# Kernel optimization log

Hardware: AMD Instinct MI355X
Metric: run time of the kernel (lower is better)

The kernel has to match this reference:

```python
import jax, jax.numpy as jnp
import numpy as np

N = 262144  # capacity (number of stored key/value rows)
D = 512     # key/query dim
V = 512     # value dim


def setup_inputs() -> dict:
    key = jax.random.key(0)
    k1, k2, k3 = jax.random.split(key, 3)
    query = jax.random.normal(k1, (D,), dtype=jnp.float32)
    keys = jax.random.normal(k2, (N, D), dtype=jnp.float32)
    values = jax.random.normal(k3, (N, V), dtype=jnp.float32)
    return {"query": query, "keys": keys, "values": values}


def reference(query, keys, values):
    # logits: [N] = keys @ query
    logits = jnp.einsum("nd,d->n", keys, query)
    attention = jax.nn.softmax(logits, axis=0)  # [N]
    # hard top-1 mask: keep only the entries equal to the max (usually one)
    mask = attention >= jnp.max(attention)      # bool, non-differentiable
    attention = mask * attention
    out = jnp.einsum("n,nv->v", attention, values)  # [V]
    return out
```

## Files before the change

### kernel.cpp

```cpp
#include <hip/hip_runtime.h>
#include <float.h>
#include <math.h>

#define DIM 512
#define VDIM 512
#define ROWS_PER_WAVE 32
#define WAVES_PER_BLOCK 4

__global__ __launch_bounds__(256) void logits_partials(
    const float* __restrict__ query,
    const float* __restrict__ keys,
    int n,
    float* __restrict__ pmax,
    float* __restrict__ psum,
    int*   __restrict__ pidx)
{
    const int lane = threadIdx.x & 63;
    const int wave = threadIdx.x >> 6;

    const float4 q0 = *(const float4*)(query + lane * 8);
    const float4 q1 = *(const float4*)(query + lane * 8 + 4);

    const int waveId = blockIdx.x * WAVES_PER_BLOCK + wave;
    const int row0   = waveId * ROWS_PER_WAVE;

    float m  = -FLT_MAX;
    float s  = 0.0f;
    int   mi = -1;

    for (int r = 0; r < ROWS_PER_WAVE; ++r) {
        const int row = row0 + r;
        if (row >= n) break;
        const float* kp = keys + (size_t)row * DIM + lane * 8;
        const float4 k0 = *(const float4*)kp;
        const float4 k1 = *(const float4*)(kp + 4);
        float d = k0.x*q0.x + k0.y*q0.y + k0.z*q0.z + k0.w*q0.w
                + k1.x*q1.x + k1.y*q1.y + k1.z*q1.z + k1.w*q1.w;
        #pragma unroll
        for (int off = 32; off > 0; off >>= 1)
            d += __shfl_xor(d, off, 64);
        if (d > m) {
            s = s * expf(m - d) + 1.0f;
            m = d;
            mi = row;
        } else {
            s += expf(d - m);
        }
    }

    __shared__ float sm[WAVES_PER_BLOCK];
    __shared__ float ss[WAVES_PER_BLOCK];
    __shared__ int   si[WAVES_PER_BLOCK];
    if (lane == 0) { sm[wave] = m; ss[wave] = s; si[wave] = mi; }
    __syncthreads();
    if (threadIdx.x == 0) {
        float M = sm[0]; int I = si[0];
        #pragma unroll
        for (int w = 1; w < WAVES_PER_BLOCK; ++w)
            if (sm[w] > M) { M = sm[w]; I = si[w]; }
        float S = 0.0f;
        #pragma unroll
        for (int w = 0; w < WAVES_PER_BLOCK; ++w)
            S += ss[w] * expf(sm[w] - M);
        pmax[blockIdx.x] = M;
        psum[blockIdx.x] = S;
        pidx[blockIdx.x] = I;
    }
}

__global__ __launch_bounds__(512) void finalize(
    const float* __restrict__ pmax,
    const float* __restrict__ psum,
    const int*   __restrict__ pidx,
    int nb,
    const float* __restrict__ values,
    float* __restrict__ out)
{
    __shared__ float sm[512];
    __shared__ int   si[512];
    __shared__ float ssum[512];

    const int tid = threadIdx.x;

    float m = -FLT_MAX; int mi = -1;
    for (int b = tid; b < nb; b += 512) {
        const float mb = pmax[b];
        if (mb > m) { m = mb; mi = pidx[b]; }
    }
    sm[tid] = m; si[tid] = mi;
    __syncthreads();
    #pragma unroll
    for (int off = 256; off > 0; off >>= 1) {
        if (tid < off) {
            if (sm[tid + off] > sm[tid]) { sm[tid] = sm[tid + off]; si[tid] = si[tid + off]; }
        }
        __syncthreads();
    }
    const float M = sm[0];
    const int   I = si[0];

    float s = 0.0f;
    for (int b = tid; b < nb; b += 512)
        s += psum[b] * expf(pmax[b] - M);
    ssum[tid] = s;
    __syncthreads();
    #pragma unroll
    for (int off = 256; off > 0; off >>= 1) {
        if (tid < off) ssum[tid] += ssum[tid + off];
        __syncthreads();
    }
    const float inv = 1.0f / ssum[0];

    for (int v = tid; v < VDIM; v += 512)
        out[v] = values[(size_t)I * VDIM + v] * inv;
}

extern "C" void kernel_launch(void* const* d_in, const int* in_sizes, int n_in,
                              void* d_out, int out_size, void* d_ws, size_t ws_size,
                              hipStream_t stream) {
    const float* query  = (const float*)d_in[0];
    const float* keys   = (const float*)d_in[1];
    const float* values = (const float*)d_in[2];
    float* out = (float*)d_out;

    const int n = in_sizes[1] / DIM;

    const int rowsPerBlock = ROWS_PER_WAVE * WAVES_PER_BLOCK;
    const int nb = (n + rowsPerBlock - 1) / rowsPerBlock;

    float* pmax = (float*)d_ws;
    float* psum = pmax + nb;
    int*   pidx = (int*)(psum + nb);

    logits_partials<<<nb, 256, 0, stream>>>(query, keys, n, pmax, psum, pidx);
    finalize<<<1, 512, 0, stream>>>(pmax, psum, pidx, nb, values, out);
}
```

Baseline: 887.5 us.

## Software-pipeline key loads in chunks of four rows with coalesced float4 layout

The logits kernel now processes each wave's rows in chunks of four and prefetches the next chunk's keys into registers while computing the current one. Each lane reads two float4s at offsets lane*4 and 256+lane*4, so every wave-wide load instruction covers a contiguous span. The four shuffle reductions are interleaved, and the online softmax update is rewritten branch-free with a single exp per row. The aim is more memory-level parallelism on a bandwidth-bound 512 MB stream, at the cost of extra registers.

```diff
diff --git a/kernel.cpp b/kernel.cpp
--- a/kernel.cpp
+++ b/kernel.cpp
@@ -6,6 +6,8 @@
 #define VDIM 512
 #define ROWS_PER_WAVE 32
 #define WAVES_PER_BLOCK 4
+#define CHUNK 4
+#define NCHUNK (ROWS_PER_WAVE / CHUNK)
 
 __global__ __launch_bounds__(256) void logits_partials(
     const float* __restrict__ query,
@@ -18,8 +20,8 @@
     const int lane = threadIdx.x & 63;
     const int wave = threadIdx.x >> 6;
 
-    const float4 q0 = *(const float4*)(query + lane * 8);
-    const float4 q1 = *(const float4*)(query + lane * 8 + 4);
+    const float4 q0 = *(const float4*)(query + lane * 4);
+    const float4 q1 = *(const float4*)(query + 256 + lane * 4);
 
     const int waveId = blockIdx.x * WAVES_PER_BLOCK + wave;
     const int row0   = waveId * ROWS_PER_WAVE;
@@ -28,23 +30,78 @@
     float s  = 0.0f;
     int   mi = -1;
 
-    for (int r = 0; r < ROWS_PER_WAVE; ++r) {
-        const int row = row0 + r;
-        if (row >= n) break;
-        const float* kp = keys + (size_t)row * DIM + lane * 8;
-        const float4 k0 = *(const float4*)kp;
-        const float4 k1 = *(const float4*)(kp + 4);
-        float d = k0.x*q0.x + k0.y*q0.y + k0.z*q0.z + k0.w*q0.w
-                + k1.x*q1.x + k1.y*q1.y + k1.z*q1.z + k1.w*q1.w;
+    if (row0 + ROWS_PER_WAVE <= n) {
+        const float* kp = keys + (size_t)row0 * DIM;
+
+        float4 ka[CHUNK], kb[CHUNK];
         #pragma unroll
-        for (int off = 32; off > 0; off >>= 1)
-            d += __shfl_xor(d, off, 64);
-        if (d > m) {
-            s = s * expf(m - d) + 1.0f;
-            m = d;
-            mi = row;
-        } else {
-            s += expf(d - m);
+        for (int r = 0; r < CHUNK; ++r) {
+            ka[r] = *(const float4*)(kp + r * DIM + lane * 4);
+            kb[r] = *(const float4*)(kp + r * DIM + 256 + lane * 4);
+        }
+
+        int rowc = row0;
+        #pragma unroll 1
+        for (int c = 0; c < NCHUNK; ++c) {
+            float4 na[CHUNK], nb[CHUNK];
+            const bool more = (c + 1 < NCHUNK);
+            if (more) {
+                const float* np = kp + (c + 1) * CHUNK * DIM;
+                #pragma unroll
+                for (int r = 0; r < CHUNK; ++r) {
+                    na[r] = *(const float4*)(np + r * DIM + lane * 4);
+                    nb[r] = *(const float4*)(np + r * DIM + 256 + lane * 4);
+                }
+            }
+
+            float d[CHUNK];
+            #pragma unroll
+            for (int r = 0; r < CHUNK; ++r)
+                d[r] = ka[r].x*q0.x + ka[r].y*q0.y + ka[r].z*q0.z + ka[r].w*q0.w
+                     + kb[r].x*q1.x + kb[r].y*q1.y + kb[r].z*q1.z + kb[r].w*q1.w;
+
+            #pragma unroll
+            for (int off = 32; off > 0; off >>= 1) {
+                #pragma unroll
+                for (int r = 0; r < CHUNK; ++r)
+                    d[r] += __shfl_xor(d[r], off, 64);
+            }
+
+            #pragma unroll
+            for (int r = 0; r < CHUNK; ++r) {
+                const float dv = d[r];
+                const float dm = fmaxf(m, dv);
+                const float e  = expf(fminf(m, dv) - dm);
+                const bool  g  = dv > m;
+                s  = g ? fmaf(s, e, 1.0f) : (s + e);
+                mi = g ? (rowc + r) : mi;
+                m  = dm;
+            }
+            rowc += CHUNK;
+
+            if (more) {
+                #pragma unroll
+                for (int r = 0; r < CHUNK; ++r) { ka[r] = na[r]; kb[r] = nb[r]; }
+            }
+        }
+    } else {
+        for (int r = 0; r < ROWS_PER_WAVE; ++r) {
+            const int row = row0 + r;
+            if (row >= n) break;
+            const float* kp = keys + (size_t)row * DIM;
+            const float4 k0 = *(const float4*)(kp + lane * 4);
+            const float4 k1 = *(const float4*)(kp + 256 + lane * 4);
+            float d = k0.x*q0.x + k0.y*q0.y + k0.z*q0.z + k0.w*q0.w
+                    + k1.x*q1.x + k1.y*q1.y + k1.z*q1.z + k1.w*q1.w;
+            #pragma unroll
+            for (int off = 32; off > 0; off >>= 1)
+                d += __shfl_xor(d, off, 64);
+            const float dm = fmaxf(m, d);
+            const float e  = expf(fminf(m, d) - dm);
+            const bool  g  = d > m;
+            s  = g ? fmaf(s, e, 1.0f) : (s + e);
+            mi = g ? row : mi;
+            m  = dm;
         }
     }
 
```

After: 881.1 us. Within noise of the previous version (-0.7%).

## Process four rows per wave concurrently with batched loads and fewer shuffles

Applied to the files above, without the earlier changes.

Splits each wave into four 16-lane groups, so each group handles one row at a time and each lane covers eight 4-float chunks of the query. The 32 rows per wave are loaded as 8 independent float4 loads per step, and the cross-lane reduction shrinks to 4 shuffle stages over 16 lanes. Online softmax merging is then done per lane and combined across groups. This raises memory-level parallelism and cuts the serialized per-row shuffle and exp chain, at the cost of more registers.

```diff
diff --git a/kernel.cpp b/kernel.cpp
--- a/kernel.cpp
+++ b/kernel.cpp
@@ -17,35 +17,90 @@
 {
     const int lane = threadIdx.x & 63;
     const int wave = threadIdx.x >> 6;
+    const int sub  = lane & 15;
+    const int rg   = lane >> 4;
 
-    const float4 q0 = *(const float4*)(query + lane * 8);
-    const float4 q1 = *(const float4*)(query + lane * 8 + 4);
+    float4 q[8];
+    #pragma unroll
+    for (int p = 0; p < 8; ++p)
+        q[p] = *(const float4*)(query + p * 64 + sub * 4);
 
     const int waveId = blockIdx.x * WAVES_PER_BLOCK + wave;
     const int row0   = waveId * ROWS_PER_WAVE;
 
-    float m  = -FLT_MAX;
-    float s  = 0.0f;
-    int   mi = -1;
+    float acc[8];
+    #pragma unroll
+    for (int g = 0; g < 8; ++g) acc[g] = 0.0f;
 
-    for (int r = 0; r < ROWS_PER_WAVE; ++r) {
-        const int row = row0 + r;
-        if (row >= n) break;
-        const float* kp = keys + (size_t)row * DIM + lane * 8;
-        const float4 k0 = *(const float4*)kp;
-        const float4 k1 = *(const float4*)(kp + 4);
-        float d = k0.x*q0.x + k0.y*q0.y + k0.z*q0.z + k0.w*q0.w
-                + k1.x*q1.x + k1.y*q1.y + k1.z*q1.z + k1.w*q1.w;
+    bool rowValid[8];
+    #pragma unroll
+    for (int g = 0; g < 8; ++g) rowValid[g] = true;
+
+    if (row0 + ROWS_PER_WAVE <= n) {
+        const float* kbase = keys + (size_t)row0 * DIM + (size_t)rg * DIM + sub * 4;
         #pragma unroll
-        for (int off = 32; off > 0; off >>= 1)
-            d += __shfl_xor(d, off, 64);
-        if (d > m) {
-            s = s * expf(m - d) + 1.0f;
-            m = d;
-            mi = row;
-        } else {
-            s += expf(d - m);
+        for (int p = 0; p < 8; ++p) {
+            float4 k[8];
+            #pragma unroll
+            for (int g = 0; g < 8; ++g)
+                k[g] = *(const float4*)(kbase + g * (4 * DIM) + p * 64);
+            #pragma unroll
+            for (int g = 0; g < 8; ++g) {
+                acc[g] = fmaf(k[g].x, q[p].x, acc[g]);
+                acc[g] = fmaf(k[g].y, q[p].y, acc[g]);
+                acc[g] = fmaf(k[g].z, q[p].z, acc[g]);
+                acc[g] = fmaf(k[g].w, q[p].w, acc[g]);
+            }
         }
+    } else {
+        #pragma unroll
+        for (int g = 0; g < 8; ++g) {
+            const int row = row0 + g * 4 + rg;
+            if (row < n) {
+                const float* kp = keys + (size_t)row * DIM + sub * 4;
+                #pragma unroll
+                for (int p = 0; p < 8; ++p) {
+                    const float4 k = *(const float4*)(kp + p * 64);
+                    acc[g] = fmaf(k.x, q[p].x, acc[g]);
+                    acc[g] = fmaf(k.y, q[p].y, acc[g]);
+                    acc[g] = fmaf(k.z, q[p].z, acc[g]);
+                    acc[g] = fmaf(k.w, q[p].w, acc[g]);
+                }
+            } else {
+                rowValid[g] = false;
+            }
+        }
+    }
+
+    #pragma unroll
+    for (int off = 1; off < 16; off <<= 1) {
+        #pragma unroll
+        for (int g = 0; g < 8; ++g)
+            acc[g] += __shfl_xor(acc[g], off, 64);
+    }
+
+    float m = -FLT_MAX, s = 0.0f;
+    int mi = -1;
+    #pragma unroll
+    for (int g = 0; g < 8; ++g) {
+        const float dv = rowValid[g] ? acc[g] : -FLT_MAX;
+        const float dm = fmaxf(m, dv);
+        const float e  = expf(fminf(m, dv) - dm);
+        const bool  gt = dv > m;
+        s  = gt ? fmaf(s, e, 1.0f) : (s + e);
+        mi = gt ? (row0 + g * 4 + rg) : mi;
+        m  = dm;
+    }
+
+    #pragma unroll
+    for (int off = 16; off <= 32; off <<= 1) {
+        const float m2 = __shfl_xor(m, off, 64);
+        const float s2 = __shfl_xor(s, off, 64);
+        const int  mi2 = __shfl_xor(mi, off, 64);
+        const float M  = fmaxf(m, m2);
+        const float S  = s * expf(m - M) + s2 * expf(m2 - M);
+        mi = (m2 > m || (m2 == m && mi2 >= 0 && (mi < 0 || mi2 < mi))) ? mi2 : mi;
+        m = M; s = S;
     }
 
     __shared__ float sm[WAVES_PER_BLOCK];
```

After: 879.8 us. Within noise of the previous version (-0.9%).
